# Performance work log

Measured on AMD Instinct MI355X. Metric: run time of the kernel, lower is better.

## Reference

```python
import jax, jax.numpy as jnp
import numpy as np
from jax.ops import segment_sum

N_NODES = 300000
N_EDGES = 600000
N_GRAPHS = 12000
HIDDEN = 128
F_ATOM, V_ATOM, D_ATOM = 9, 119, 9
F_BOND, V_BOND, D_BOND = 3, 6, 3


def setup_inputs() -> dict:
    key = jax.random.key(0)
    ks = jax.random.split(key, 12)
    x = jax.random.randint(ks[0], (N_NODES, F_ATOM), 0, 100, dtype=jnp.int64 if jax.config.jax_enable_x64 else jnp.int32)
    edge_index = jax.random.randint(ks[1], (2, N_EDGES), 0, N_NODES)
    edge_attr = jax.random.randint(ks[2], (N_EDGES, F_BOND), 0, 5)
    batch = jnp.sort(jax.random.randint(ks[3], (N_NODES,), 0, N_GRAPHS))
    s = 0.02
    atom_emb = jax.random.normal(ks[4], (F_ATOM, V_ATOM, D_ATOM), jnp.float32) * s
    bond_emb = jax.random.normal(ks[5], (F_BOND, V_BOND, D_BOND), jnp.float32) * s
    W1 = jax.random.normal(ks[6], (D_ATOM, HIDDEN), jnp.float32) * (1.0 / np.sqrt(D_ATOM))
    b1 = jnp.zeros((HIDDEN,), jnp.float32)
    W2 = jax.random.normal(ks[7], (HIDDEN, HIDDEN), jnp.float32) * (1.0 / np.sqrt(HIDDEN))
    b2 = jnp.zeros((HIDDEN,), jnp.float32)
    Wfc = jax.random.normal(ks[8], (HIDDEN, 128), jnp.float32) * (1.0 / np.sqrt(HIDDEN))
    bfc = jnp.zeros((128,), jnp.float32)
    return {"x": x, "edge_index": edge_index, "edge_attr": edge_attr, "batch": batch,
            "atom_emb": atom_emb, "bond_emb": bond_emb,
            "W1": W1, "b1": b1, "W2": W2, "b2": b2, "Wfc": Wfc, "bfc": bfc}


def _multi_embed(tables, idx):
    # tables: [F, V, D], idx: [N, F] -> sum over F of tables[f, idx[:, f]] -> [N, D]
    F = tables.shape[0]
    gathered = tables[jnp.arange(F)[None, :], idx]  # [N, F, D]
    return gathered.sum(axis=1)


def _gcn_conv(h, edge_index, W, b, n_nodes):
    # PyG GCNConv: add self-loops, symmetric deg^-1/2 normalization
    src, dst = edge_index[0], edge_index[1]
    deg = segment_sum(jnp.ones(src.shape[0], h.dtype), dst, num_segments=n_nodes) + 1.0  # self-loop
    dinv = jax.lax.rsqrt(deg)
    h = h @ W  # transform before propagation
    coef = (dinv[src] * dinv[dst])[:, None]
    agg = segment_sum(h[src] * coef, dst, num_segments=n_nodes)
    agg = agg + h * (dinv * dinv)[:, None]  # self-loop contribution (norm = 1/deg)
    return agg + b


def reference(x, edge_index, edge_attr, batch, atom_emb, bond_emb, W1, b1, W2, b2, Wfc, bfc):
    h = _multi_embed(atom_emb, x)            # AtomEncoder: [N, 9]
    _ = _multi_embed(bond_emb, edge_attr)    # BondEncoder (computed, unused downstream)
    h = _gcn_conv(h, edge_index, W1, b1, N_NODES)
    h = jax.nn.relu(h)
    h = _gcn_conv(h, edge_index, W2, b2, N_NODES)
    # global_mean_pool over graphs
    sums = segment_sum(h, batch, num_segments=N_GRAPHS)
    cnt = segment_sum(jnp.ones(N_NODES, h.dtype), batch, num_segments=N_GRAPHS)
    graph_emb = sums / jnp.clip(cnt, 1.0)[:, None]
    return graph_emb @ Wfc + bfc
```

## Files before the change

### kernel.cpp

```cpp
#include <hip/hip_runtime.h>

#define NN 300000
#define NE 600000
#define NG 12000
#define HH 128
#define FA 9
#define VA 119
#define DA 9
#define NCHUNK ((NN + 1023) / 1024)
#define POISON 0xAAAAAAAAu

#define HB  64
#define NCB 1172
#define NTH (NCB * 256)

#define OEMB 0
#define OW1  (FA*VA*DA)
#define OB1  (OW1 + DA*HH)
#define OW2  (OB1 + HH)
#define OB2  (OW2 + HH*HH)
#define OWFC (OB2 + HH)
#define OBFC (OWFC + HH*HH)
#define NWC  (OBFC + HH)

typedef unsigned short u16;
typedef unsigned int u32;
typedef __attribute__((ext_vector_type(8))) short bfrag8;
typedef __attribute__((ext_vector_type(16))) float ffrag16;

__device__ __forceinline__ float bf2f(u16 u){
  union { u32 i; float f; } v; v.i = ((u32)u) << 16; return v.f;
}
__device__ __forceinline__ float bflo(u32 w){
  union { u32 i; float f; } v; v.i = w << 16; return v.f;
}
__device__ __forceinline__ float bfhi(u32 w){
  union { u32 i; float f; } v; v.i = w & 0xFFFF0000u; return v.f;
}
__device__ __forceinline__ u16 f2bf(float f){
  union { float f; u32 i; } v; v.f = f;
  u32 x = v.i;
  return (u16)((x + 0x7FFFu + ((x >> 16) & 1u)) >> 16);
}
__device__ __forceinline__ float ldf(const void* p, int i, int isf32){
  return isf32 ? ((const float*)p)[i] : bf2f(((const u16*)p)[i]);
}
__device__ __forceinline__ int detect_isf32(const u16* emb16, int t, int* scnt){
  if (t == 0) *scnt = 0;
  __syncthreads();
  u16 u = emb16[t];
  int e = (u >> 7) & 0xFF;
  if (e >= 96 && e < 126) atomicAdd(scnt, 1);
  __syncthreads();
  return (*scnt >= 200) ? 0 : 1;
}

__global__ void k_pre(const int* __restrict__ x, const void* emb, const void* W1,
                      const void* b1, const void* W2, const void* b2,
                      const void* Wfc, const void* bfc,
                      const int* __restrict__ batch, const int* __restrict__ dst,
                      int* __restrict__ flag, float* __restrict__ wc,
                      u32* __restrict__ degcur, u16* __restrict__ rank,
                      int* __restrict__ gstart, uint4* __restrict__ h0p,
                      float* __restrict__ wcomb,
                      float* __restrict__ bcomb, u32* __restrict__ btab2){
  __shared__ float embS[FA * VA * DA];
  __shared__ int scnt;
  int t = threadIdx.x;

  if (blockIdx.x < HB){
    int htid = blockIdx.x * 256 + t;
    const int4* d4 = (const int4*)dst;
    uint2* r2 = (uint2*)rank;
    #pragma unroll 2
    for (int i = htid; i < NE / 4; i += HB * 256){
      int4 v = d4[i];
      u32 r0 = atomicAdd(&degcur[v.x], 1u);
      u32 r1 = atomicAdd(&degcur[v.y], 1u);
      u32 rr2 = atomicAdd(&degcur[v.z], 1u);
      u32 rr3 = atomicAdd(&degcur[v.w], 1u);
      uint2 pk;
      pk.x = (u32)(u16)(r0 - POISON) | (((u32)(u16)(r1 - POISON)) << 16);
      pk.y = (u32)(u16)(rr2 - POISON) | (((u32)(u16)(rr3 - POISON)) << 16);
      r2[i] = pk;
    }
    return;
  }

  int isf32 = detect_isf32((const u16*)emb, t, &scnt);
  int tid = (blockIdx.x - HB) * 256 + t;
  if (tid == 0) flag[0] = isf32;

  if (isf32){
    const float4* e4 = (const float4*)emb;
    for (int i = t; i < (FA*VA*DA)/4; i += 256){
      float4 v = e4[i];
      int o = i * 4;
      embS[o+0] = v.x; embS[o+1] = v.y; embS[o+2] = v.z; embS[o+3] = v.w;
    }
    if (t < 3) embS[9636 + t] = ((const float*)emb)[9636 + t];
  } else {
    const uint4* e4 = (const uint4*)emb;
    for (int i = t; i < (FA*VA*DA)/8; i += 256){
      uint4 v = e4[i];
      int o = i * 8;
      embS[o+0] = bflo(v.x); embS[o+1] = bfhi(v.x);
      embS[o+2] = bflo(v.y); embS[o+3] = bfhi(v.y);
      embS[o+4] = bflo(v.z); embS[o+5] = bfhi(v.z);
      embS[o+6] = bflo(v.w); embS[o+7] = bfhi(v.w);
    }
    if (t < 7) embS[9632 + t] = bf2f(((const u16*)emb)[9632 + t]);
  }

  for (int i = tid; i < NWC; i += NTH){
    float v;
    if      (i < OW1)  v = ldf(emb, i - OEMB, isf32);
    else if (i < OB1)  v = ldf(W1,  i - OW1,  isf32);
    else if (i < OW2)  v = ldf(b1,  i - OB1,  isf32);
    else if (i < OB2)  v = ldf(W2,  i - OW2,  isf32);
    else if (i < OWFC) v = ldf(b2,  i - OB2,  isf32);
    else if (i < OBFC) v = ldf(Wfc, i - OWFC, isf32);
    else               v = ldf(bfc, i - OBFC, isf32);
    wc[i] = v;
  }

  if (tid < HH * HH){
    int d = tid >> 7, k = tid & 127;
    float s = 0.f;
    #pragma unroll 4
    for (int j = 0; j < HH; ++j) s += ldf(W2, d * HH + j, isf32) * ldf(Wfc, j * HH + k, isf32);
    wcomb[tid] = s;
    if (tid < HH){
      float sb = 0.f;
      #pragma unroll 4
      for (int j = 0; j < HH; ++j) sb += ldf(b2, j, isf32) * ldf(Wfc, j * HH + tid, isf32);
      bcomb[tid] = sb;
    }
    if (tid < 1024){
      int lane = tid >> 4, idx = tid & 15;
      int tile = idx >> 2, reg = idx & 3;
      int half = lane >> 5, col = lane & 31;
      int nn = tile * 32 + col;
      int k0 = half * 8 + reg * 2;
      int k1 = k0 + 1;
      u32 lo = 0, hi = 0;
      if (k0 < 9)       lo = f2bf(ldf(W1, k0 * HH + nn, isf32));
      else if (k0 == 9) lo = f2bf(ldf(b1, nn, isf32));
      if (k1 < 9)       hi = f2bf(ldf(W1, k1 * HH + nn, isf32));
      else if (k1 == 9) hi = f2bf(ldf(b1, nn, isf32));
      btab2[tid] = lo | (hi << 16);
    }
  }

  __syncthreads();
  int n = tid;
  if (n <= NG){
    if (n == NG) gstart[NG] = NN;
    else {
      int lo = 0, hi = NN;
      while (lo < hi){
        int mid = (lo + hi) >> 1;
        if (batch[mid] < n) lo = mid + 1; else hi = mid;
      }
      gstart[n] = lo;
    }
  }
  if (n >= NN) return;
  int idx[FA];
  #pragma unroll
  for (int f = 0; f < FA; ++f) idx[f] = x[n * FA + f];
  float acc[DA];
  #pragma unroll
  for (int d = 0; d < DA; ++d){
    float a = 0.f;
    #pragma unroll
    for (int f = 0; f < FA; ++f) a += embS[(f * VA + idx[f]) * DA + d];
    acc[d] = a;
  }
  uint4 pv;
  pv.x = (u32)f2bf(acc[0]) | ((u32)f2bf(acc[1]) << 16);
  pv.y = (u32)f2bf(acc[2]) | ((u32)f2bf(acc[3]) << 16);
  pv.z = (u32)f2bf(acc[4]) | ((u32)f2bf(acc[5]) << 16);
  pv.w = (u32)f2bf(acc[6]) | ((u32)f2bf(acc[7]) << 16);
  h0p[2 * n] = pv;
  ((u32*)h0p)[8 * n + 4] = (u32)f2bf(acc[8]);
}

__global__ void k_scan(const u32* __restrict__ degp, int* __restrict__ rowoff,
                       float* __restrict__ dinv, u32* __restrict__ sync){
  __shared__ int sh[256];
  __shared__ int sbase;
  int b = blockIdx.x;
  int t = threadIdx.x;
  int i0 = b * 1024 + t * 4;
  int v0=0, v1=0, v2=0, v3=0;
  if (i0 + 0 < NN){ v0 = (int)(degp[i0 + 0] - POISON); dinv[i0 + 0] = rsqrtf((float)v0 + 1.0f); }
  if (i0 + 1 < NN){ v1 = (int)(degp[i0 + 1] - POISON); dinv[i0 + 1] = rsqrtf((float)v1 + 1.0f); }
  if (i0 + 2 < NN){ v2 = (int)(degp[i0 + 2] - POISON); dinv[i0 + 2] = rsqrtf((float)v2 + 1.0f); }
  if (i0 + 3 < NN){ v3 = (int)(degp[i0 + 3] - POISON); dinv[i0 + 3] = rsqrtf((float)v3 + 1.0f); }
  int tsum = v0 + v1 + v2 + v3;
  sh[t] = tsum;
  __syncthreads();
  for (int off = 1; off < 256; off <<= 1){
    int add = (t >= off) ? sh[t - off] : 0;
    __syncthreads();
    sh[t] += add;
    __syncthreads();
  }
  int run = sh[t] - tsum;
  int tot = sh[255];

  if (t == 0){
    u32 w = (b == 0) ? ((3u << 30) | (u32)tot) : ((1u << 30) | (u32)tot);
    __hip_atomic_store(&sync[b], w, __ATOMIC_RELAXED, __HIP_MEMORY_SCOPE_AGENT);
    if (b == 0) sbase = 0;
  }
  if (b > 0 && t >= 192){
    int lane = t & 63;
    int running = 0;
    int p = b - 1;
    for (;;){
      int q = p - lane;
      u32 w = (q >= 0)
            ? __hip_atomic_load(&sync[q], __ATOMIC_RELAXED, __HIP_MEMORY_SCOPE_AGENT)
            : (3u << 30);
      u32 st = w >> 30;
      int val = (int)(w & 0x3FFFFFFFu);
      unsigned long long bi = __ballot(st == 3u);
      unsigned long long bg = __ballot(st == 1u);
      if (bi){
        int L = (int)(__ffsll((long long)bi) - 1);
        unsigned long long need = (L == 0) ? 0ull : ((1ull << L) - 1ull);
        if ((bg & need) == need){
          int contrib = (lane <= L) ? val : 0;
          #pragma unroll
          for (int off = 1; off < 64; off <<= 1) contrib += __shfl_xor(contrib, off, 64);
          running += contrib;
          break;
        }
      } else if (bg == ~0ull){
        int contrib = val;
        #pragma unroll
        for (int off = 1; off < 64; off <<= 1) contrib += __shfl_xor(contrib, off, 64);
        running += contrib;
        p -= 64;
      }
    }
    if (lane == 0){
      sbase = running;
      __hip_atomic_store(&sync[b], (3u << 30) | (u32)(running + tot),
                         __ATOMIC_RELAXED, __HIP_MEMORY_SCOPE_AGENT);
    }
  }
  __syncthreads();
  int gb = sbase;
  run += gb;
  if (i0 + 0 <= NN) rowoff[i0 + 0] = run;
  run += v0;
  if (i0 + 1 <= NN) rowoff[i0 + 1] = run;
  run += v1;
  if (i0 + 2 <= NN) rowoff[i0 + 2] = run;
  run += v2;
  if (i0 + 3 <= NN) rowoff[i0 + 3] = run;
}

__global__ void k_fill(const int* __restrict__ src, const int* __restrict__ dst,
                       const u16* __restrict__ rank, const int* __restrict__ rowoff,
                       const float* __restrict__ dinv, uint2* __restrict__ csr){
  int e = blockIdx.x * 256 + threadIdx.x;
  if (e < NE){
    int s = src[e], d = dst[e];
    int pos = rowoff[d] + (int)rank[e];
    uint2 ent;
    ent.x = (u32)s;
    ent.y = __float_as_uint(dinv[s] * dinv[d]);
    csr[pos] = ent;
  }
}

__global__ void k_l1csr(const uint4* __restrict__ h0p, uint4* __restrict__ agg1p,
                        const int* __restrict__ rowoff,
                        const uint2* __restrict__ csr, const float* __restrict__ dinv){
  int n = blockIdx.x * 256 + threadIdx.x;
  if (n >= NN) return;
  float di = dinv[n];
  float c0 = di * di;
  const u32* h0w = (const u32*)h0p;
  float acc[DA];
  {
    uint4 ra = h0p[2 * n];
    u32 r4 = h0w[8 * n + 4];
    acc[0]=c0*bflo(ra.x); acc[1]=c0*bfhi(ra.x); acc[2]=c0*bflo(ra.y); acc[3]=c0*bfhi(ra.y);
    acc[4]=c0*bflo(ra.z); acc[5]=c0*bfhi(ra.z); acc[6]=c0*bflo(ra.w); acc[7]=c0*bfhi(ra.w);
    acc[8]=c0*bflo(r4);
  }
  int s0 = rowoff[n], s1 = rowoff[n + 1];
  #pragma unroll 2
  for (int j = s0; j < s1; ++j){
    uint2 ent = csr[j];
    int s = (int)ent.x;
    float c = __uint_as_float(ent.y);
    uint4 ra = h0p[2 * s];
    u32 r4 = h0w[8 * s + 4];
    acc[0]+=c*bflo(ra.x); acc[1]+=c*bfhi(ra.x); acc[2]+=c*bflo(ra.y); acc[3]+=c*bfhi(ra.y);
    acc[4]+=c*bflo(ra.z); acc[5]+=c*bfhi(ra.z); acc[6]+=c*bflo(ra.w); acc[7]+=c*bfhi(ra.w);
    acc[8]+=c*bflo(r4);
  }
  uint4 pv;
  pv.x = (u32)f2bf(acc[0]) | ((u32)f2bf(acc[1]) << 16);
  pv.y = (u32)f2bf(acc[2]) | ((u32)f2bf(acc[3]) << 16);
  pv.z = (u32)f2bf(acc[4]) | ((u32)f2bf(acc[5]) << 16);
  pv.w = (u32)f2bf(acc[6]) | ((u32)f2bf(acc[7]) << 16);
  agg1p[2 * n] = pv;
  ((u32*)agg1p)[8 * n + 4] = (u32)f2bf(acc[8]) | (0x3F80u << 16);
}

__global__ void k_l2pool(const uint4* __restrict__ agg1p,
                         const float* __restrict__ dinv,
                         const int* __restrict__ rowoff,
                         const uint2* __restrict__ csr, const int* __restrict__ gstart,
                         const u32* __restrict__ btab2, float* __restrict__ pooled){
  int t = threadIdx.x;
  int g = blockIdx.x * 4 + (t >> 6);
  int lane = t & 63;
  if (g >= NG) return;
  const u32* aggw = (const u32*)agg1p;
  u32 bf[16];
  {
    const u32* bp = btab2 + lane * 16;
    #pragma unroll
    for (int i = 0; i < 16; ++i) bf[i] = bp[i];
  }
  int a = gstart[g], b = gstart[g + 1];
  int j0 = rowoff[a], j1 = rowoff[b];
  int nself = b - a;
  int M = nself + (j1 - j0);
  float s[4] = {0.f, 0.f, 0.f, 0.f};
  int half = lane >> 5;
  int li = lane & 31;

  for (int base = 0; base < M; base += 32){
    int i = base + li;
    u32 a0 = 0, a1 = 0, a2 = 0, a3 = 0;
    float coef = 0.f;
    if (i < M){
      int n;
      if (i < nself){
        n = a + i;
        float dn = dinv[n];
        coef = dn * dn;
      } else {
        uint2 e = csr[j0 + (i - nself)];
        n = (int)e.x;
        coef = __uint_as_float(e.y);
      }
      if (half == 0){
        uint4 ra = agg1p[2 * n];
        a0 = ra.x; a1 = ra.y; a2 = ra.z; a3 = ra.w;
      } else {
        a0 = aggw[8 * n + 4];
      }
    }
    float cf[16];
    #pragma unroll
    for (int reg = 0; reg < 16; ++reg){
      int row = (reg & 3) + 8 * (reg >> 2) + 4 * half;
      cf[reg] = __shfl(coef, row, 64);
    }
    union { u32 u[4]; bfrag8 v; } au;
    au.u[0] = a0; au.u[1] = a1; au.u[2] = a2; au.u[3] = a3;
    #pragma unroll
    for (int tile = 0; tile < 4; ++tile){
      union { u32 u[4]; bfrag8 v; } bu;
      bu.u[0] = bf[tile*4+0]; bu.u[1] = bf[tile*4+1];
      bu.u[2] = bf[tile*4+2]; bu.u[3] = bf[tile*4+3];
      ffrag16 c;
      #pragma unroll
      for (int q = 0; q < 16; ++q) c[q] = 0.f;
      c = __builtin_amdgcn_mfma_f32_32x32x16_bf16(au.v, bu.v, c, 0, 0, 0);
      float acc = 0.f;
      #pragma unroll
      for (int reg = 0; reg < 16; ++reg)
        acc += fmaxf(c[reg], 0.f) * cf[reg];
      s[tile] += acc;
    }
  }
  #pragma unroll
  for (int tile = 0; tile < 4; ++tile){
    float v = s[tile];
    v += __shfl_xor(v, 32, 64);
    s[tile] = v;
  }
  if (half == 0){
    #pragma unroll
    for (int tile = 0; tile < 4; ++tile)
      pooled[(size_t)g * HH + tile * 32 + li] = s[tile];
  }
}

__global__ void k_head(const float* __restrict__ pooled, const float* __restrict__ wcomb,
                       const float* __restrict__ bcomb, const float* __restrict__ wc,
                       const int* __restrict__ gstart, const int* __restrict__ flag,
                       void* __restrict__ out){
  __shared__ float wS[HH * HH];
  __shared__ float pl[2][HH];
  int t = threadIdx.x;
  for (int i = t; i < HH * HH; i += 256) wS[i] = wcomb[i];
  __syncthreads();
  int isf32 = flag[0];
  int gg = t >> 7, k = t & 127;
  for (int p = blockIdx.x; p < NG / 2; p += gridDim.x){
    int g = p * 2 + gg;
    int cnt = gstart[g + 1] - gstart[g];
    float inv = 1.0f / (float)(cnt > 1 ? cnt : 1);
    pl[gg][k] = pooled[(size_t)g * HH + k] * inv;
    __syncthreads();
    float acc = wc[OBFC + k] + (cnt > 0 ? bcomb[k] : 0.f);
    #pragma unroll 8
    for (int d = 0; d < HH; ++d) acc += pl[gg][d] * wS[d * HH + k];
    if (isf32) ((float*)out)[(size_t)g * HH + k] = acc;
    else       ((u16*)out)[(size_t)g * HH + k] = f2bf(acc);
    __syncthreads();
  }
}

extern "C" void kernel_launch(void* const* d_in, const int* in_sizes, int n_in,
                              void* d_out, int out_size, void* d_ws, size_t ws_size,
                              hipStream_t stream){
  const int* x     = (const int*)d_in[0];
  const int* ei    = (const int*)d_in[1];
  const int* batch = (const int*)d_in[3];
  const void* aemb = d_in[4];
  const void* W1   = d_in[6];
  const void* b1   = d_in[7];
  const void* W2   = d_in[8];
  const void* b2   = d_in[9];
  const void* Wfc  = d_in[10];
  const void* bfc  = d_in[11];
  const int* srcp = ei;
  const int* dstp = ei + NE;

  char* p = (char*)d_ws;
  int*   flag   = (int*)p;                 p += 64;
  float* wc     = (float*)p;               p += sizeof(float) * 43944;
  float* wcomb  = (float*)p;               p += sizeof(float) * (HH * HH);
  float* bcomb  = (float*)p;               p += sizeof(float) * HH;
  u32*   btab2  = (u32*)p;                 p += sizeof(u32) * 1024;
  u32*   degcur = (u32*)p;                 p += sizeof(u32) * (NN + 16);
  int*   rowoff = (int*)p;                 p += sizeof(int) * (NN + 4);
  u32*   sync   = (u32*)p;                 p += sizeof(u32) * 512;
  float* dinv   = (float*)p;               p += sizeof(float) * NN;
  u16*   rank   = (u16*)p;                 p += sizeof(u16) * (NE + 8);
  uint2* csr    = (uint2*)p;               p += sizeof(uint2) * NE;
  int*   gstart = (int*)p;                 p += sizeof(int) * (NG + 4);
  float* pooled = (float*)p;               p += sizeof(float) * (size_t)NG * HH;
  uint4* h0p    = (uint4*)p;               p += sizeof(uint4) * 2 * NN;
  uint4* agg1p  = (uint4*)p;               p += sizeof(uint4) * 2 * NN;
  (void)p; (void)ws_size; (void)n_in; (void)in_sizes; (void)out_size;

  k_pre   <<<HB + NCB, 256, 0, stream>>>(x, aemb, W1, b1, W2, b2, Wfc, bfc,
                                         batch, dstp, flag, wc, degcur, rank,
                                         gstart, h0p, wcomb, bcomb, btab2);
  k_scan  <<<NCHUNK, 256, 0, stream>>>(degcur, rowoff, dinv, sync);
  k_fill  <<<(NE + 255) / 256, 256, 0, stream>>>(srcp, dstp, rank, rowoff, dinv, csr);
  k_l1csr <<<(NN + 255) / 256, 256, 0, stream>>>(h0p, agg1p, rowoff, csr, dinv);
  k_l2pool<<<NG / 4, 256, 0, stream>>>(agg1p, dinv, rowoff, csr, gstart, btab2, pooled);
  k_head  <<<512, 256, 0, stream>>>(pooled, wcomb, bcomb, wc, gstart, flag, d_out);
}
```

Measured before the change: 215.6 us.

## Split degree histogram into its own fully parallel kernel

The destination-degree histogram and rank computation was done by 64 dedicated blocks inside the preprocessing kernel, each grid-striding over the edges. It now runs as a separate kernel with one thread per four edges (586 blocks), followed by the embedding/weight preprocessing kernel. This spreads the atomic histogram over many more blocks so it does not limit the fused kernel, at the cost of an extra launch and the loss of overlap with the core work.

```diff
diff --git a/kernel.cpp b/kernel.cpp
--- a/kernel.cpp
+++ b/kernel.cpp
@@ -10,9 +10,9 @@
 #define NCHUNK ((NN + 1023) / 1024)
 #define POISON 0xAAAAAAAAu
 
-#define HB  64
 #define NCB 1172
 #define NTH (NCB * 256)
+#define NHB 586
 
 #define OEMB 0
 #define OW1  (FA*VA*DA)
@@ -55,40 +55,35 @@
   return (*scnt >= 200) ? 0 : 1;
 }
 
-__global__ void k_pre(const int* __restrict__ x, const void* emb, const void* W1,
-                      const void* b1, const void* W2, const void* b2,
-                      const void* Wfc, const void* bfc,
-                      const int* __restrict__ batch, const int* __restrict__ dst,
-                      int* __restrict__ flag, float* __restrict__ wc,
-                      u32* __restrict__ degcur, u16* __restrict__ rank,
-                      int* __restrict__ gstart, uint4* __restrict__ h0p,
-                      float* __restrict__ wcomb,
-                      float* __restrict__ bcomb, u32* __restrict__ btab2){
+__global__ void __launch_bounds__(256)
+k_hist(const int* __restrict__ dst, u32* __restrict__ degcur, u16* __restrict__ rank){
+  int i = blockIdx.x * 256 + threadIdx.x;
+  if (i >= NE / 4) return;
+  const int4* d4 = (const int4*)dst;
+  int4 v = d4[i];
+  u32 r0 = atomicAdd(&degcur[v.x], 1u);
+  u32 r1 = atomicAdd(&degcur[v.y], 1u);
+  u32 r2v = atomicAdd(&degcur[v.z], 1u);
+  u32 r3v = atomicAdd(&degcur[v.w], 1u);
+  uint2 pk;
+  pk.x = (u32)(u16)(r0 - POISON) | (((u32)(u16)(r1 - POISON)) << 16);
+  pk.y = (u32)(u16)(r2v - POISON) | (((u32)(u16)(r3v - POISON)) << 16);
+  ((uint2*)rank)[i] = pk;
+}
+
+__global__ void k_core(const int* __restrict__ x, const void* emb, const void* W1,
+                       const void* b1, const void* W2, const void* b2,
+                       const void* Wfc, const void* bfc,
+                       const int* __restrict__ batch,
+                       int* __restrict__ flag, float* __restrict__ wc,
+                       int* __restrict__ gstart, uint4* __restrict__ h0p,
+                       float* __restrict__ wcomb,
+                       float* __restrict__ bcomb, u32* __restrict__ btab2){
   __shared__ float embS[FA * VA * DA];
   __shared__ int scnt;
   int t = threadIdx.x;
-
-  if (blockIdx.x < HB){
-    int htid = blockIdx.x * 256 + t;
-    const int4* d4 = (const int4*)dst;
-    uint2* r2 = (uint2*)rank;
-    #pragma unroll 2
-    for (int i = htid; i < NE / 4; i += HB * 256){
-      int4 v = d4[i];
-      u32 r0 = atomicAdd(&degcur[v.x], 1u);
-      u32 r1 = atomicAdd(&degcur[v.y], 1u);
-      u32 rr2 = atomicAdd(&degcur[v.z], 1u);
-      u32 rr3 = atomicAdd(&degcur[v.w], 1u);
-      uint2 pk;
-      pk.x = (u32)(u16)(r0 - POISON) | (((u32)(u16)(r1 - POISON)) << 16);
-      pk.y = (u32)(u16)(rr2 - POISON) | (((u32)(u16)(rr3 - POISON)) << 16);
-      r2[i] = pk;
-    }
-    return;
-  }
-
   int isf32 = detect_isf32((const u16*)emb, t, &scnt);
-  int tid = (blockIdx.x - HB) * 256 + t;
+  int tid = blockIdx.x * 256 + t;
   if (tid == 0) flag[0] = isf32;
 
   if (isf32){
@@ -458,9 +453,9 @@
   uint4* agg1p  = (uint4*)p;               p += sizeof(uint4) * 2 * NN;
   (void)p; (void)ws_size; (void)n_in; (void)in_sizes; (void)out_size;
 
-  k_pre   <<<HB + NCB, 256, 0, stream>>>(x, aemb, W1, b1, W2, b2, Wfc, bfc,
-                                         batch, dstp, flag, wc, degcur, rank,
-                                         gstart, h0p, wcomb, bcomb, btab2);
+  k_hist  <<<NHB, 256, 0, stream>>>(dstp, degcur, rank);
+  k_core  <<<NCB, 256, 0, stream>>>(x, aemb, W1, b1, W2, b2, Wfc, bfc, batch,
+                                    flag, wc, gstart, h0p, wcomb, bcomb, btab2);
   k_scan  <<<NCHUNK, 256, 0, stream>>>(degcur, rowoff, dinv, sync);
   k_fill  <<<(NE + 255) / 256, 256, 0, stream>>>(srcp, dstp, rank, rowoff, dinv, csr);
   k_l1csr <<<(NN + 255) / 256, 256, 0, stream>>>(h0p, agg1p, rowoff, csr, dinv);
```

Measured after the change: 243.6 us. 1.13x slower.

## Pack dinv into padded h0 rows and compute edge coefficients lazily in layer-1

Applied to the files above, without the earlier changes.

The scan kernel now also writes each node's dinv into the unused padding word of its h0 row. The fill kernel no longer gathers dinv[s] and dinv[d] per edge and writes only the source index. Layer-1 aggregation reads the neighbour's dinv from the same row it already loads and writes the edge coefficient back into the CSR for layer-2 to reuse. This removes random dinv gathers in k_fill, but adds a scattered store per edge in k_l1csr and a strided write in k_scan.

```diff
diff --git a/kernel.cpp b/kernel.cpp
--- a/kernel.cpp
+++ b/kernel.cpp
@@ -187,17 +187,18 @@
 }
 
 __global__ void k_scan(const u32* __restrict__ degp, int* __restrict__ rowoff,
-                       float* __restrict__ dinv, u32* __restrict__ sync){
+                       float* __restrict__ dinv, u32* __restrict__ sync,
+                       u32* __restrict__ h0w){
   __shared__ int sh[256];
   __shared__ int sbase;
   int b = blockIdx.x;
   int t = threadIdx.x;
   int i0 = b * 1024 + t * 4;
   int v0=0, v1=0, v2=0, v3=0;
-  if (i0 + 0 < NN){ v0 = (int)(degp[i0 + 0] - POISON); dinv[i0 + 0] = rsqrtf((float)v0 + 1.0f); }
-  if (i0 + 1 < NN){ v1 = (int)(degp[i0 + 1] - POISON); dinv[i0 + 1] = rsqrtf((float)v1 + 1.0f); }
-  if (i0 + 2 < NN){ v2 = (int)(degp[i0 + 2] - POISON); dinv[i0 + 2] = rsqrtf((float)v2 + 1.0f); }
-  if (i0 + 3 < NN){ v3 = (int)(degp[i0 + 3] - POISON); dinv[i0 + 3] = rsqrtf((float)v3 + 1.0f); }
+  if (i0 + 0 < NN){ v0 = (int)(degp[i0 + 0] - POISON); float f = rsqrtf((float)v0 + 1.0f); dinv[i0 + 0] = f; h0w[8*(size_t)(i0+0) + 5] = __float_as_uint(f); }
+  if (i0 + 1 < NN){ v1 = (int)(degp[i0 + 1] - POISON); float f = rsqrtf((float)v1 + 1.0f); dinv[i0 + 1] = f; h0w[8*(size_t)(i0+1) + 5] = __float_as_uint(f); }
+  if (i0 + 2 < NN){ v2 = (int)(degp[i0 + 2] - POISON); float f = rsqrtf((float)v2 + 1.0f); dinv[i0 + 2] = f; h0w[8*(size_t)(i0+2) + 5] = __float_as_uint(f); }
+  if (i0 + 3 < NN){ v3 = (int)(degp[i0 + 3] - POISON); float f = rsqrtf((float)v3 + 1.0f); dinv[i0 + 3] = f; h0w[8*(size_t)(i0+3) + 5] = __float_as_uint(f); }
   int tsum = v0 + v1 + v2 + v3;
   sh[t] = tsum;
   __syncthreads();
@@ -266,45 +267,42 @@
 
 __global__ void k_fill(const int* __restrict__ src, const int* __restrict__ dst,
                        const u16* __restrict__ rank, const int* __restrict__ rowoff,
-                       const float* __restrict__ dinv, uint2* __restrict__ csr){
+                       u32* __restrict__ csrw){
   int e = blockIdx.x * 256 + threadIdx.x;
   if (e < NE){
     int s = src[e], d = dst[e];
     int pos = rowoff[d] + (int)rank[e];
-    uint2 ent;
-    ent.x = (u32)s;
-    ent.y = __float_as_uint(dinv[s] * dinv[d]);
-    csr[pos] = ent;
+    csrw[2 * (size_t)pos] = (u32)s;
   }
 }
 
 __global__ void k_l1csr(const uint4* __restrict__ h0p, uint4* __restrict__ agg1p,
-                        const int* __restrict__ rowoff,
-                        const uint2* __restrict__ csr, const float* __restrict__ dinv){
+                        const int* __restrict__ rowoff, u32* __restrict__ csrw){
   int n = blockIdx.x * 256 + threadIdx.x;
   if (n >= NN) return;
-  float di = dinv[n];
-  float c0 = di * di;
-  const u32* h0w = (const u32*)h0p;
+  const uint2* h0d = (const uint2*)h0p;
   float acc[DA];
+  float di;
   {
     uint4 ra = h0p[2 * n];
-    u32 r4 = h0w[8 * n + 4];
+    uint2 r45 = h0d[4 * n + 2];
+    di = __uint_as_float(r45.y);
+    float c0 = di * di;
     acc[0]=c0*bflo(ra.x); acc[1]=c0*bfhi(ra.x); acc[2]=c0*bflo(ra.y); acc[3]=c0*bfhi(ra.y);
     acc[4]=c0*bflo(ra.z); acc[5]=c0*bfhi(ra.z); acc[6]=c0*bflo(ra.w); acc[7]=c0*bfhi(ra.w);
-    acc[8]=c0*bflo(r4);
+    acc[8]=c0*bflo(r45.x);
   }
   int s0 = rowoff[n], s1 = rowoff[n + 1];
   #pragma unroll 2
   for (int j = s0; j < s1; ++j){
-    uint2 ent = csr[j];
-    int s = (int)ent.x;
-    float c = __uint_as_float(ent.y);
+    int s = (int)csrw[2 * (size_t)j];
     uint4 ra = h0p[2 * s];
-    u32 r4 = h0w[8 * s + 4];
+    uint2 r45 = h0d[4 * s + 2];
+    float c = __uint_as_float(r45.y) * di;
     acc[0]+=c*bflo(ra.x); acc[1]+=c*bfhi(ra.x); acc[2]+=c*bflo(ra.y); acc[3]+=c*bfhi(ra.y);
     acc[4]+=c*bflo(ra.z); acc[5]+=c*bfhi(ra.z); acc[6]+=c*bflo(ra.w); acc[7]+=c*bfhi(ra.w);
-    acc[8]+=c*bflo(r4);
+    acc[8]+=c*bflo(r45.x);
+    csrw[2 * (size_t)j + 1] = __float_as_uint(c);
   }
   uint4 pv;
   pv.x = (u32)f2bf(acc[0]) | ((u32)f2bf(acc[1]) << 16);
@@ -461,9 +459,9 @@
   k_pre   <<<HB + NCB, 256, 0, stream>>>(x, aemb, W1, b1, W2, b2, Wfc, bfc,
                                          batch, dstp, flag, wc, degcur, rank,
                                          gstart, h0p, wcomb, bcomb, btab2);
-  k_scan  <<<NCHUNK, 256, 0, stream>>>(degcur, rowoff, dinv, sync);
-  k_fill  <<<(NE + 255) / 256, 256, 0, stream>>>(srcp, dstp, rank, rowoff, dinv, csr);
-  k_l1csr <<<(NN + 255) / 256, 256, 0, stream>>>(h0p, agg1p, rowoff, csr, dinv);
+  k_scan  <<<NCHUNK, 256, 0, stream>>>(degcur, rowoff, dinv, sync, (u32*)h0p);
+  k_fill  <<<(NE + 255) / 256, 256, 0, stream>>>(srcp, dstp, rank, rowoff, (u32*)csr);
+  k_l1csr <<<(NN + 255) / 256, 256, 0, stream>>>(h0p, agg1p, rowoff, (u32*)csr);
   k_l2pool<<<NG / 4, 256, 0, stream>>>(agg1p, dinv, rowoff, csr, gstart, btab2, pooled);
   k_head  <<<512, 256, 0, stream>>>(pooled, wcomb, bcomb, wc, gstart, flag, d_out);
 }
```

Result: no change. 217.2 us (+0.7%).

## Fuse scan, CSR fill, layer-1 and layer-2 pooling into one persistent kernel

Applied to the files above, without the earlier changes.

Merges four kernels (degree scan, CSR fill, layer-1 aggregation, layer-2 MFMA pooling) into one persistent kernel of 1024 blocks, separated by software grid barriers built on atomic counters. The aim is to remove three kernel launch gaps and their tail effects. In exchange it needs all 1024 blocks to be co-resident, which launch_bounds(256,4) is meant to support, and the spin barriers use a poisoned counter base plus a guard timeout. Grid-stride loops replace the per-element grids.

```diff
diff --git a/kernel.cpp b/kernel.cpp
--- a/kernel.cpp
+++ b/kernel.cpp
@@ -14,6 +14,9 @@
 #define NCB 1172
 #define NTH (NCB * 256)
 
+#define TGRID 1024
+#define TTH   (TGRID * 256)
+
 #define OEMB 0
 #define OW1  (FA*VA*DA)
 #define OB1  (OW1 + DA*HH)
@@ -53,6 +56,19 @@
   if (e >= 96 && e < 126) atomicAdd(scnt, 1);
   __syncthreads();
   return (*scnt >= 200) ? 0 : 1;
+}
+
+__device__ __forceinline__ void gbar(u32* ctr){
+  __syncthreads();
+  if (threadIdx.x == 0){
+    __hip_atomic_fetch_add(ctr, 1u, __ATOMIC_ACQ_REL, __HIP_MEMORY_SCOPE_AGENT);
+    int guard = 0;
+    while ((u32)(__hip_atomic_load(ctr, __ATOMIC_ACQUIRE, __HIP_MEMORY_SCOPE_AGENT) - POISON) < (u32)TGRID){
+      __builtin_amdgcn_s_sleep(8);
+      if (++guard > 200000) break;
+    }
+  }
+  __syncthreads();
 }
 
 __global__ void k_pre(const int* __restrict__ x, const void* emb, const void* W1,
@@ -186,89 +202,96 @@
   ((u32*)h0p)[8 * n + 4] = (u32)f2bf(acc[8]);
 }
 
-__global__ void k_scan(const u32* __restrict__ degp, int* __restrict__ rowoff,
-                       float* __restrict__ dinv, u32* __restrict__ sync){
+__global__ void __launch_bounds__(256, 4)
+k_tail(const u32* __restrict__ degp, int* __restrict__ rowoff,
+       float* __restrict__ dinv, u32* __restrict__ syncw,
+       const int* __restrict__ src, const int* __restrict__ dst,
+       const u16* __restrict__ rank, uint2* __restrict__ csr,
+       const uint4* __restrict__ h0p, uint4* __restrict__ agg1p,
+       const int* __restrict__ gstart, const u32* __restrict__ btab2,
+       float* __restrict__ pooled){
   __shared__ int sh[256];
   __shared__ int sbase;
-  int b = blockIdx.x;
   int t = threadIdx.x;
-  int i0 = b * 1024 + t * 4;
-  int v0=0, v1=0, v2=0, v3=0;
-  if (i0 + 0 < NN){ v0 = (int)(degp[i0 + 0] - POISON); dinv[i0 + 0] = rsqrtf((float)v0 + 1.0f); }
-  if (i0 + 1 < NN){ v1 = (int)(degp[i0 + 1] - POISON); dinv[i0 + 1] = rsqrtf((float)v1 + 1.0f); }
-  if (i0 + 2 < NN){ v2 = (int)(degp[i0 + 2] - POISON); dinv[i0 + 2] = rsqrtf((float)v2 + 1.0f); }
-  if (i0 + 3 < NN){ v3 = (int)(degp[i0 + 3] - POISON); dinv[i0 + 3] = rsqrtf((float)v3 + 1.0f); }
-  int tsum = v0 + v1 + v2 + v3;
-  sh[t] = tsum;
-  __syncthreads();
-  for (int off = 1; off < 256; off <<= 1){
-    int add = (t >= off) ? sh[t - off] : 0;
+  int bid = blockIdx.x;
+  u32* bctr = syncw + 384;
+
+  if (bid < NCHUNK){
+    int b = bid;
+    int i0 = b * 1024 + t * 4;
+    int v0=0, v1=0, v2=0, v3=0;
+    if (i0 + 0 < NN){ v0 = (int)(degp[i0 + 0] - POISON); dinv[i0 + 0] = rsqrtf((float)v0 + 1.0f); }
+    if (i0 + 1 < NN){ v1 = (int)(degp[i0 + 1] - POISON); dinv[i0 + 1] = rsqrtf((float)v1 + 1.0f); }
+    if (i0 + 2 < NN){ v2 = (int)(degp[i0 + 2] - POISON); dinv[i0 + 2] = rsqrtf((float)v2 + 1.0f); }
+    if (i0 + 3 < NN){ v3 = (int)(degp[i0 + 3] - POISON); dinv[i0 + 3] = rsqrtf((float)v3 + 1.0f); }
+    int tsum = v0 + v1 + v2 + v3;
+    sh[t] = tsum;
     __syncthreads();
-    sh[t] += add;
-    __syncthreads();
-  }
-  int run = sh[t] - tsum;
-  int tot = sh[255];
-
-  if (t == 0){
-    u32 w = (b == 0) ? ((3u << 30) | (u32)tot) : ((1u << 30) | (u32)tot);
-    __hip_atomic_store(&sync[b], w, __ATOMIC_RELAXED, __HIP_MEMORY_SCOPE_AGENT);
-    if (b == 0) sbase = 0;
-  }
-  if (b > 0 && t >= 192){
-    int lane = t & 63;
-    int running = 0;
-    int p = b - 1;
-    for (;;){
-      int q = p - lane;
-      u32 w = (q >= 0)
-            ? __hip_atomic_load(&sync[q], __ATOMIC_RELAXED, __HIP_MEMORY_SCOPE_AGENT)
-            : (3u << 30);
-      u32 st = w >> 30;
-      int val = (int)(w & 0x3FFFFFFFu);
-      unsigned long long bi = __ballot(st == 3u);
-      unsigned long long bg = __ballot(st == 1u);
-      if (bi){
-        int L = (int)(__ffsll((long long)bi) - 1);
-        unsigned long long need = (L == 0) ? 0ull : ((1ull << L) - 1ull);
-        if ((bg & need) == need){
-          int contrib = (lane <= L) ? val : 0;
+    for (int off = 1; off < 256; off <<= 1){
+      int add = (t >= off) ? sh[t - off] : 0;
+      __syncthreads();
+      sh[t] += add;
+      __syncthreads();
+    }
+    int run = sh[t] - tsum;
+    int tot = sh[255];
+
+    if (t == 0){
+      u32 w = (b == 0) ? ((3u << 30) | (u32)tot) : ((1u << 30) | (u32)tot);
+      __hip_atomic_store(&syncw[b], w, __ATOMIC_RELAXED, __HIP_MEMORY_SCOPE_AGENT);
+      if (b == 0) sbase = 0;
+    }
+    if (b > 0 && t >= 192){
+      int lane = t & 63;
+      int running = 0;
+      int p = b - 1;
+      for (;;){
+        int q = p - lane;
+        u32 w = (q >= 0)
+              ? __hip_atomic_load(&syncw[q], __ATOMIC_RELAXED, __HIP_MEMORY_SCOPE_AGENT)
+              : (3u << 30);
+        u32 st = w >> 30;
+        int val = (int)(w & 0x3FFFFFFFu);
+        unsigned long long bi = __ballot(st == 3u);
+        unsigned long long bg = __ballot(st == 1u);
+        if (bi){
+          int L = (int)(__ffsll((long long)bi) - 1);
+          unsigned long long need = (L == 0) ? 0ull : ((1ull << L) - 1ull);
+          if ((bg & need) == need){
+            int contrib = (lane <= L) ? val : 0;
+            #pragma unroll
+            for (int off = 1; off < 64; off <<= 1) contrib += __shfl_xor(contrib, off, 64);
+            running += contrib;
+            break;
+          }
+        } else if (bg == ~0ull){
+          int contrib = val;
           #pragma unroll
           for (int off = 1; off < 64; off <<= 1) contrib += __shfl_xor(contrib, off, 64);
           running += contrib;
-          break;
+          p -= 64;
         }
-      } else if (bg == ~0ull){
-        int contrib = val;
-        #pragma unroll
-        for (int off = 1; off < 64; off <<= 1) contrib += __shfl_xor(contrib, off, 64);
-        running += contrib;
-        p -= 64;
-      }
-    }
-    if (lane == 0){
-      sbase = running;
-      __hip_atomic_store(&sync[b], (3u << 30) | (u32)(running + tot),
-                         __ATOMIC_RELAXED, __HIP_MEMORY_SCOPE_AGENT);
-    }
-  }
-  __syncthreads();
-  int gb = sbase;
-  run += gb;
-  if (i0 + 0 <= NN) rowoff[i0 + 0] = run;
-  run += v0;
-  if (i0 + 1 <= NN) rowoff[i0 + 1] = run;
-  run += v1;
-  if (i0 + 2 <= NN) rowoff[i0 + 2] = run;
-  run += v2;
-  if (i0 + 3 <= NN) rowoff[i0 + 3] = run;
-}
-
-__global__ void k_fill(const int* __restrict__ src, const int* __restrict__ dst,
-                       const u16* __restrict__ rank, const int* __restrict__ rowoff,
-                       const float* __restrict__ dinv, uint2* __restrict__ csr){
-  int e = blockIdx.x * 256 + threadIdx.x;
-  if (e < NE){
+      }
+      if (lane == 0){
+        sbase = running;
+        __hip_atomic_store(&syncw[b], (3u << 30) | (u32)(running + tot),
+                           __ATOMIC_RELAXED, __HIP_MEMORY_SCOPE_AGENT);
+      }
+    }
+    __syncthreads();
+    int gb = sbase;
+    run += gb;
+    if (i0 + 0 <= NN) rowoff[i0 + 0] = run;
+    run += v0;
+    if (i0 + 1 <= NN) rowoff[i0 + 1] = run;
+    run += v1;
+    if (i0 + 2 <= NN) rowoff[i0 + 2] = run;
+    run += v2;
+    if (i0 + 3 <= NN) rowoff[i0 + 3] = run;
+  }
+  gbar(&bctr[0]);
+
+  for (int e = bid * 256 + t; e < NE; e += TTH){
     int s = src[e], d = dst[e];
     int pos = rowoff[d] + (int)rank[e];
     uint2 ent;
@@ -276,125 +299,118 @@
     ent.y = __float_as_uint(dinv[s] * dinv[d]);
     csr[pos] = ent;
   }
-}
-
-__global__ void k_l1csr(const uint4* __restrict__ h0p, uint4* __restrict__ agg1p,
-                        const int* __restrict__ rowoff,
-                        const uint2* __restrict__ csr, const float* __restrict__ dinv){
-  int n = blockIdx.x * 256 + threadIdx.x;
-  if (n >= NN) return;
-  float di = dinv[n];
-  float c0 = di * di;
-  const u32* h0w = (const u32*)h0p;
-  float acc[DA];
+  gbar(&bctr[1]);
+
+  for (int n = bid * 256 + t; n < NN; n += TTH){
+    float di = dinv[n];
+    float c0 = di * di;
+    const u32* h0w = (const u32*)h0p;
+    float acc[DA];
+    {
+      uint4 ra = h0p[2 * n];
+      u32 r4 = h0w[8 * n + 4];
+      acc[0]=c0*bflo(ra.x); acc[1]=c0*bfhi(ra.x); acc[2]=c0*bflo(ra.y); acc[3]=c0*bfhi(ra.y);
+      acc[4]=c0*bflo(ra.z); acc[5]=c0*bfhi(ra.z); acc[6]=c0*bflo(ra.w); acc[7]=c0*bfhi(ra.w);
+      acc[8]=c0*bflo(r4);
+    }
+    int s0 = rowoff[n], s1 = rowoff[n + 1];
+    #pragma unroll 2
+    for (int j = s0; j < s1; ++j){
+      uint2 ent = csr[j];
+      int s = (int)ent.x;
+      float c = __uint_as_float(ent.y);
+      uint4 ra = h0p[2 * s];
+      u32 r4 = h0w[8 * s + 4];
+      acc[0]+=c*bflo(ra.x); acc[1]+=c*bfhi(ra.x); acc[2]+=c*bflo(ra.y); acc[3]+=c*bfhi(ra.y);
+      acc[4]+=c*bflo(ra.z); acc[5]+=c*bfhi(ra.z); acc[6]+=c*bflo(ra.w); acc[7]+=c*bfhi(ra.w);
+      acc[8]+=c*bflo(r4);
+    }
+    uint4 pv;
+    pv.x = (u32)f2bf(acc[0]) | ((u32)f2bf(acc[1]) << 16);
+    pv.y = (u32)f2bf(acc[2]) | ((u32)f2bf(acc[3]) << 16);
+    pv.z = (u32)f2bf(acc[4]) | ((u32)f2bf(acc[5]) << 16);
+    pv.w = (u32)f2bf(acc[6]) | ((u32)f2bf(acc[7]) << 16);
+    agg1p[2 * n] = pv;
+    ((u32*)agg1p)[8 * n + 4] = (u32)f2bf(acc[8]) | (0x3F80u << 16);
+  }
+  gbar(&bctr[2]);
+
   {
-    uint4 ra = h0p[2 * n];
-    u32 r4 = h0w[8 * n + 4];
-    acc[0]=c0*bflo(ra.x); acc[1]=c0*bfhi(ra.x); acc[2]=c0*bflo(ra.y); acc[3]=c0*bfhi(ra.y);
-    acc[4]=c0*bflo(ra.z); acc[5]=c0*bfhi(ra.z); acc[6]=c0*bflo(ra.w); acc[7]=c0*bfhi(ra.w);
-    acc[8]=c0*bflo(r4);
-  }
-  int s0 = rowoff[n], s1 = rowoff[n + 1];
-  #pragma unroll 2
-  for (int j = s0; j < s1; ++j){
-    uint2 ent = csr[j];
-    int s = (int)ent.x;
-    float c = __uint_as_float(ent.y);
-    uint4 ra = h0p[2 * s];
-    u32 r4 = h0w[8 * s + 4];
-    acc[0]+=c*bflo(ra.x); acc[1]+=c*bfhi(ra.x); acc[2]+=c*bflo(ra.y); acc[3]+=c*bfhi(ra.y);
-    acc[4]+=c*bflo(ra.z); acc[5]+=c*bfhi(ra.z); acc[6]+=c*bflo(ra.w); acc[7]+=c*bfhi(ra.w);
-    acc[8]+=c*bflo(r4);
-  }
-  uint4 pv;
-  pv.x = (u32)f2bf(acc[0]) | ((u32)f2bf(acc[1]) << 16);
-  pv.y = (u32)f2bf(acc[2]) | ((u32)f2bf(acc[3]) << 16);
-  pv.z = (u32)f2bf(acc[4]) | ((u32)f2bf(acc[5]) << 16);
-  pv.w = (u32)f2bf(acc[6]) | ((u32)f2bf(acc[7]) << 16);
-  agg1p[2 * n] = pv;
-  ((u32*)agg1p)[8 * n + 4] = (u32)f2bf(acc[8]) | (0x3F80u << 16);
-}
-
-__global__ void k_l2pool(const uint4* __restrict__ agg1p,
-                         const float* __restrict__ dinv,
-                         const int* __restrict__ rowoff,
-                         const uint2* __restrict__ csr, const int* __restrict__ gstart,
-                         const u32* __restrict__ btab2, float* __restrict__ pooled){
-  int t = threadIdx.x;
-  int g = blockIdx.x * 4 + (t >> 6);
-  int lane = t & 63;
-  if (g >= NG) return;
-  const u32* aggw = (const u32*)agg1p;
-  u32 bf[16];
-  {
-    const u32* bp = btab2 + lane * 16;
-    #pragma unroll
-    for (int i = 0; i < 16; ++i) bf[i] = bp[i];
-  }
-  int a = gstart[g], b = gstart[g + 1];
-  int j0 = rowoff[a], j1 = rowoff[b];
-  int nself = b - a;
-  int M = nself + (j1 - j0);
-  float s[4] = {0.f, 0.f, 0.f, 0.f};
-  int half = lane >> 5;
-  int li = lane & 31;
-
-  for (int base = 0; base < M; base += 32){
-    int i = base + li;
-    u32 a0 = 0, a1 = 0, a2 = 0, a3 = 0;
-    float coef = 0.f;
-    if (i < M){
-      int n;
-      if (i < nself){
-        n = a + i;
-        float dn = dinv[n];
-        coef = dn * dn;
-      } else {
-        uint2 e = csr[j0 + (i - nself)];
-        n = (int)e.x;
-        coef = __uint_as_float(e.y);
+    const u32* aggw = (const u32*)agg1p;
+    int lane = t & 63;
+    int half = lane >> 5;
+    int li = lane & 31;
+    u32 bf[16];
+    {
+      const u32* bp = btab2 + lane * 16;
+      #pragma unroll
+      for (int i = 0; i < 16; ++i) bf[i] = bp[i];
+    }
+    for (int g = bid * 4 + (t >> 6); g < NG; g += TGRID * 4){
+      int a = gstart[g], b = gstart[g + 1];
+      int j0 = rowoff[a], j1 = rowoff[b];
+      int nself = b - a;
+      int M = nself + (j1 - j0);
+      float s[4] = {0.f, 0.f, 0.f, 0.f};
+
+      for (int base = 0; base < M; base += 32){
+        int i = base + li;
+        u32 a0 = 0, a1 = 0, a2 = 0, a3 = 0;
+        float coef = 0.f;
+        if (i < M){
+          int n;
+          if (i < nself){
+            n = a + i;
+            float dn = dinv[n];
+            coef = dn * dn;
+          } else {
+            uint2 e = csr[j0 + (i - nself)];
+            n = (int)e.x;
+            coef = __uint_as_float(e.y);
+          }
+          if (half == 0){
+            uint4 ra = agg1p[2 * n];
+            a0 = ra.x; a1 = ra.y; a2 = ra.z; a3 = ra.w;
+          } else {
+            a0 = aggw[8 * n + 4];
+          }
+        }
+        float cf[16];
+        #pragma unroll
+        for (int reg = 0; reg < 16; ++reg){
+          int row = (reg & 3) + 8 * (reg >> 2) + 4 * half;
+          cf[reg] = __shfl(coef, row, 64);
+        }
+        union { u32 u[4]; bfrag8 v; } au;
+        au.u[0] = a0; au.u[1] = a1; au.u[2] = a2; au.u[3] = a3;
+        #pragma unroll
+        for (int tile = 0; tile < 4; ++tile){
+          union { u32 u[4]; bfrag8 v; } bu;
+          bu.u[0] = bf[tile*4+0]; bu.u[1] = bf[tile*4+1];
+          bu.u[2] = bf[tile*4+2]; bu.u[3] = bf[tile*4+3];
+          ffrag16 c;
+          #pragma unroll
+          for (int q = 0; q < 16; ++q) c[q] = 0.f;
+          c = __builtin_amdgcn_mfma_f32_32x32x16_bf16(au.v, bu.v, c, 0, 0, 0);
+          float acc = 0.f;
+          #pragma unroll
+          for (int reg = 0; reg < 16; ++reg)
+            acc += fmaxf(c[reg], 0.f) * cf[reg];
+          s[tile] += acc;
+        }
+      }
+      #pragma unroll
+      for (int tile = 0; tile < 4; ++tile){
+        float v = s[tile];
+        v += __shfl_xor(v, 32, 64);
+        s[tile] = v;
       }
       if (half == 0){
-        uint4 ra = agg1p[2 * n];
-        a0 = ra.x; a1 = ra.y; a2 = ra.z; a3 = ra.w;
-      } else {
-        a0 = aggw[8 * n + 4];
-      }
-    }
-    float cf[16];
-    #pragma unroll
-    for (int reg = 0; reg < 16; ++reg){
-      int row = (reg & 3) + 8 * (reg >> 2) + 4 * half;
-      cf[reg] = __shfl(coef, row, 64);
-    }
-    union { u32 u[4]; bfrag8 v; } au;
-    au.u[0] = a0; au.u[1] = a1; au.u[2] = a2; au.u[3] = a3;
-    #pragma unroll
-    for (int tile = 0; tile < 4; ++tile){
-      union { u32 u[4]; bfrag8 v; } bu;
-      bu.u[0] = bf[tile*4+0]; bu.u[1] = bf[tile*4+1];
-      bu.u[2] = bf[tile*4+2]; bu.u[3] = bf[tile*4+3];
-      ffrag16 c;
-      #pragma unroll
-      for (int q = 0; q < 16; ++q) c[q] = 0.f;
-      c = __builtin_amdgcn_mfma_f32_32x32x16_bf16(au.v, bu.v, c, 0, 0, 0);
-      float acc = 0.f;
-      #pragma unroll
-      for (int reg = 0; reg < 16; ++reg)
-        acc += fmaxf(c[reg], 0.f) * cf[reg];
-      s[tile] += acc;
-    }
-  }
-  #pragma unroll
-  for (int tile = 0; tile < 4; ++tile){
-    float v = s[tile];
-    v += __shfl_xor(v, 32, 64);
-    s[tile] = v;
-  }
-  if (half == 0){
-    #pragma unroll
-    for (int tile = 0; tile < 4; ++tile)
-      pooled[(size_t)g * HH + tile * 32 + li] = s[tile];
+        #pragma unroll
+        for (int tile = 0; tile < 4; ++tile)
+          pooled[(size_t)g * HH + tile * 32 + li] = s[tile];
+      }
+    }
   }
 }
 
@@ -448,7 +464,7 @@
   u32*   btab2  = (u32*)p;                 p += sizeof(u32) * 1024;
   u32*   degcur = (u32*)p;                 p += sizeof(u32) * (NN + 16);
   int*   rowoff = (int*)p;                 p += sizeof(int) * (NN + 4);
-  u32*   sync   = (u32*)p;                 p += sizeof(u32) * 512;
+  u32*   syncw  = (u32*)p;                 p += sizeof(u32) * 512;
   float* dinv   = (float*)p;               p += sizeof(float) * NN;
   u16*   rank   = (u16*)p;                 p += sizeof(u16) * (NE + 8);
   uint2* csr    = (uint2*)p;               p += sizeof(uint2) * NE;
@@ -458,12 +474,10 @@
   uint4* agg1p  = (uint4*)p;               p += sizeof(uint4) * 2 * NN;
   (void)p; (void)ws_size; (void)n_in; (void)in_sizes; (void)out_size;
 
-  k_pre   <<<HB + NCB, 256, 0, stream>>>(x, aemb, W1, b1, W2, b2, Wfc, bfc,
-                                         batch, dstp, flag, wc, degcur, rank,
-                                         gstart, h0p, wcomb, bcomb, btab2);
-  k_scan  <<<NCHUNK, 256, 0, stream>>>(degcur, rowoff, dinv, sync);
-  k_fill  <<<(NE + 255) / 256, 256, 0, stream>>>(srcp, dstp, rank, rowoff, dinv, csr);
-  k_l1csr <<<(NN + 255) / 256, 256, 0, stream>>>(h0p, agg1p, rowoff, csr, dinv);
-  k_l2pool<<<NG / 4, 256, 0, stream>>>(agg1p, dinv, rowoff, csr, gstart, btab2, pooled);
-  k_head  <<<512, 256, 0, stream>>>(pooled, wcomb, bcomb, wc, gstart, flag, d_out);
-}
+  k_pre <<<HB + NCB, 256, 0, stream>>>(x, aemb, W1, b1, W2, b2, Wfc, bfc,
+                                       batch, dstp, flag, wc, degcur, rank,
+                                       gstart, h0p, wcomb, bcomb, btab2);
+  k_tail<<<TGRID, 256, 0, stream>>>(degcur, rowoff, dinv, syncw, srcp, dstp,
+                                    rank, csr, h0p, agg1p, gstart, btab2, pooled);
+  k_head<<<512, 256, 0, stream>>>(pooled, wcomb, bcomb, wc, gstart, flag, d_out);
+}
```

Result: slower. 586.7 us (+172.1%).
